# Kernel tuning notes

Measured on AMD Instinct MI355X. Metric: run time of the kernel, lower is better.

The kernel has to match this reference:

```python
import jax, jax.numpy as jnp
import numpy as np

N, E = 20000, 320000
IN_CH, HID, NPRED = 64, 512, 12
NUM_GCN = 3   # num_gcn_layers=4 -> 1 + (4-2) layers
NUM_RNN = 2
BN_EPS = 1e-5


def setup_inputs() -> dict:
    key = jax.random.key(0)
    ks = jax.random.split(key, 16)
    s = 0.05  # init scale to keep activations sane
    return {
        "x": jax.random.normal(ks[0], (N, IN_CH), jnp.float32),
        "edge_index": jax.random.randint(ks[1], (2, E), 0, N, jnp.int32),
        "edge_weight": jax.random.uniform(ks[2], (E,), jnp.float32),
        "gcn0_W": jax.random.normal(ks[3], (IN_CH, HID), jnp.float32) * s,
        "gcn0_b": jnp.zeros((HID,), jnp.float32),
        "gcn_W": jax.random.normal(ks[4], (NUM_GCN - 1, HID, HID), jnp.float32) * s,
        "gcn_b": jnp.zeros((NUM_GCN - 1, HID), jnp.float32),
        "bn_gamma": jnp.ones((NUM_GCN, HID), jnp.float32),
        "bn_beta": jnp.zeros((NUM_GCN, HID), jnp.float32),
        "w_ih": jax.random.normal(ks[5], (NUM_RNN, HID, 4 * HID), jnp.float32) * s,
        "w_hh": jax.random.normal(ks[6], (NUM_RNN, HID, 4 * HID), jnp.float32) * s,
        "w_ch": jax.random.normal(ks[7], (NUM_RNN, HID, 3 * HID), jnp.float32) * s,
        "lstm_b": jnp.zeros((NUM_RNN, 4 * HID), jnp.float32),
        "out_W": jax.random.normal(ks[8], (HID, NPRED), jnp.float32) * s,
        "out_b": jnp.zeros((NPRED,), jnp.float32),
    }


def _gcn(x, W, b, src, dst, ew, n):
    h = x @ W                                   # [N, out]
    msg = ew[:, None] * h[src]                  # [E, out]
    return jax.ops.segment_sum(msg, dst, num_segments=n) + b


def _bn_relu(x, gamma, beta):
    mu = jnp.mean(x, axis=0)
    var = jnp.var(x, axis=0)
    return jax.nn.relu((x - mu) * jax.lax.rsqrt(var + BN_EPS) * gamma + beta)


def _peephole_cell(inp, h, c, Wih, Whh, Wch, b):
    H = h.shape[1]
    gates = inp @ Wih + h @ Whh + b             # [N, 4H]
    i_g, f_g, g_g, o_g = jnp.split(gates, 4, axis=1)
    g_g = g_g + c @ Wch[:, :H]
    i_g = jax.nn.sigmoid(i_g)
    f_g = jax.nn.sigmoid(f_g + c @ Wch[:, H:2 * H])
    g_g = jnp.tanh(g_g)
    cy = f_g * c + i_g * g_g
    o_g = o_g + cy @ Wch[:, 2 * H:]
    hy = jax.nn.sigmoid(o_g) * jnp.tanh(cy)
    return hy, cy


def reference(x, edge_index, edge_weight, gcn0_W, gcn0_b, gcn_W, gcn_b,
              bn_gamma, bn_beta, w_ih, w_hh, w_ch, lstm_b, out_W, out_b):
    src, dst = edge_index[0], edge_index[1]
    n = x.shape[0]
    # GCN stack: conv -> batchnorm (train-mode stats) -> relu (dropout=0)
    h = _gcn(x, gcn0_W, gcn0_b, src, dst, edge_weight, n)
    h = _bn_relu(h, bn_gamma[0], bn_beta[0])
    for i in range(NUM_GCN - 1):
        h = _gcn(h, gcn_W[i], gcn_b[i], src, dst, edge_weight, n)
        h = _bn_relu(h, bn_gamma[i + 1], bn_beta[i + 1])
    # seq_len == 1 after unsqueeze; cells chained sharing (h_t, c_t)
    h_t = jnp.zeros((n, HID), h.dtype)
    c_t = jnp.zeros((n, HID), h.dtype)
    for l in range(NUM_RNN):
        h_t, c_t = _peephole_cell(h, h_t, c_t, w_ih[l], w_hh[l], w_ch[l], lstm_b[l])
    out = h_t @ out_W + out_b                   # [N, num_predictions]
    return jnp.squeeze(out)
```

## Files before the change

### kernel.cpp

```cpp
#include <hip/hip_runtime.h>
#include <cstddef>

#define N_NODES 20000
#define N_EDGES 320000
#define IN_CH   64
#define HID     512
#define G4      2048
#define BN_EPS  1e-5f

typedef __attribute__((ext_vector_type(8))) __bf16 bf16x8;
typedef __attribute__((ext_vector_type(4))) float f32x4;

__device__ __forceinline__ float sigmoidf_(float x) {
  return 1.0f / (1.0f + expf(-x));
}

__device__ __forceinline__ unsigned short f2b(float f) {
  unsigned int u = __float_as_uint(f);
  u += 0x7FFFu + ((u >> 16) & 1u);
  return (unsigned short)(u >> 16);
}
__device__ __forceinline__ float b2f(unsigned short u) {
  return __uint_as_float(((unsigned int)u) << 16);
}

__device__ __forceinline__ void gld_lds16(const unsigned short* g, unsigned short* l) {
  __builtin_amdgcn_global_load_lds(
      (const __attribute__((address_space(1))) unsigned int*)(const void*)g,
      (__attribute__((address_space(3))) unsigned int*)(void*)l, 16, 0, 0);
}

__global__ __launch_bounds__(256) void zero_k(float* __restrict__ p, size_t n) {
  size_t i = ((size_t)blockIdx.x * 256 + threadIdx.x) * 4;
  if (i + 3 < n) {
    *(float4*)&p[i] = make_float4(0.f, 0.f, 0.f, 0.f);
  } else {
    for (; i < n; i++) p[i] = 0.f;
  }
}

__global__ __launch_bounds__(256) void cvt_k(const float* __restrict__ in,
                                             unsigned short* __restrict__ out, size_t n) {
  size_t i = ((size_t)blockIdx.x * 256 + threadIdx.x) * 4;
  if (i + 3 < n) {
    const float4 v = *(const float4*)&in[i];
    ushort4 o; o.x = f2b(v.x); o.y = f2b(v.y); o.z = f2b(v.z); o.w = f2b(v.w);
    *(ushort4*)&out[i] = o;
  } else {
    for (; i < n; i++) out[i] = f2b(in[i]);
  }
}

struct TcvtDesc { const float* W; unsigned short* Wt; int K, NC, ldw, ldo, gate; };
struct TcvtBatch { TcvtDesc d[19]; };

__global__ void tcvtb_k(TcvtBatch batch) {
  const TcvtDesc dd = batch.d[blockIdx.z];
  __shared__ float tile[32][33];
  const int n0 = blockIdx.x * 32, k0 = blockIdx.y * 32;
  if (n0 >= dd.NC || k0 >= dd.K) return;
  const int tx = threadIdx.x, ty = threadIdx.y;
  #pragma unroll
  for (int i = 0; i < 32; i += 8) {
    int k = k0 + ty + i, n = n0 + tx;
    tile[ty + i][tx] = (k < dd.K && n < dd.NC) ? dd.W[(size_t)k * dd.ldw + n] : 0.f;
  }
  __syncthreads();
  #pragma unroll
  for (int i = 0; i < 32; i += 8) {
    int n = n0 + ty + i, k = k0 + tx;
    if (n < dd.NC && k < dd.K) {
      size_t orow = (dd.gate < 0)
          ? (size_t)n
          : (size_t)((n >> 4) * 64 + dd.gate * 16 + (n & 15));
      dd.Wt[orow * dd.ldo + k] = f2b(tile[tx][ty + i]);
    }
  }
}

__global__ __launch_bounds__(256) void hist_k(const int* __restrict__ dst,
                                              int* __restrict__ counts) {
  int e = blockIdx.x * 256 + threadIdx.x;
  if (e < N_EDGES) atomicAdd(&counts[dst[e]], 1);
}

__global__ __launch_bounds__(1024) void scan_k(const int* __restrict__ counts,
                                               int* __restrict__ offsets,
                                               int* __restrict__ pos, int n) {
  __shared__ int tmp[1024];
  __shared__ int carry_s;
  const int tid = threadIdx.x;
  if (tid == 0) carry_s = 0;
  __syncthreads();
  for (int base = 0; base < n; base += 1024) {
    int i = base + tid;
    int v = (i < n) ? counts[i] : 0;
    tmp[tid] = v;
    __syncthreads();
    #pragma unroll
    for (int off = 1; off < 1024; off <<= 1) {
      int t = (tid >= off) ? tmp[tid - off] : 0;
      __syncthreads();
      tmp[tid] += t;
      __syncthreads();
    }
    if (i < n) {
      int excl = carry_s + tmp[tid] - v;
      offsets[i] = excl;
      pos[i] = excl;
    }
    __syncthreads();
    if (tid == 1023) carry_s += tmp[1023];
    __syncthreads();
  }
  if (tid == 0) offsets[n] = carry_s;
}

__global__ __launch_bounds__(256) void fill_k(
    const int* __restrict__ src, const int* __restrict__ dst,
    const float* __restrict__ ew, int* __restrict__ pos,
    int* __restrict__ s_s, float* __restrict__ w_s) {
  int e = blockIdx.x * 256 + threadIdx.x;
  if (e >= N_EDGES) return;
  int p = atomicAdd(&pos[dst[e]], 1);
  s_s[p] = src[e];
  w_s[p] = ew[e];
}

__global__ __launch_bounds__(64) void gather64_k(
    const unsigned short* __restrict__ x16, const int* __restrict__ offsets,
    const int* __restrict__ s_s, const float* __restrict__ w_s,
    unsigned short* __restrict__ xg) {
  const int sub = threadIdx.x >> 4;
  const int cg  = threadIdx.x & 15;
  const int n   = blockIdx.x * 4 + sub;
  const int beg = offsets[n], end = offsets[n + 1];
  float4 acc = make_float4(0.f, 0.f, 0.f, 0.f);
  for (int i = beg; i < end; i++) {
    const int   s = s_s[i];
    const float w = w_s[i];
    const ushort4 v = *(const ushort4*)&x16[(size_t)s * IN_CH + cg * 4];
    acc.x = fmaf(w, b2f(v.x), acc.x);
    acc.y = fmaf(w, b2f(v.y), acc.y);
    acc.z = fmaf(w, b2f(v.z), acc.z);
    acc.w = fmaf(w, b2f(v.w), acc.w);
  }
  ushort4 o; o.x = f2b(acc.x); o.y = f2b(acc.y); o.z = f2b(acc.z); o.w = f2b(acc.w);
  *(ushort4*)&xg[(size_t)n * IN_CH + cg * 4] = o;
}

__global__ __launch_bounds__(128) void gather_k(
    const unsigned short* __restrict__ XW, const int* __restrict__ offsets,
    const int* __restrict__ s_s, const float* __restrict__ w_s,
    unsigned short* __restrict__ H) {
  const int n = blockIdx.x;
  const int t = threadIdx.x;
  const int beg = offsets[n], end = offsets[n + 1];
  float4 acc = make_float4(0.f, 0.f, 0.f, 0.f);
  for (int i = beg; i < end; i++) {
    const int   s = s_s[i];
    const float w = w_s[i];
    const ushort4 v = *(const ushort4*)&XW[(size_t)s * HID + t * 4];
    acc.x = fmaf(w, b2f(v.x), acc.x);
    acc.y = fmaf(w, b2f(v.y), acc.y);
    acc.z = fmaf(w, b2f(v.z), acc.z);
    acc.w = fmaf(w, b2f(v.w), acc.w);
  }
  ushort4 o; o.x = f2b(acc.x); o.y = f2b(acc.y); o.z = f2b(acc.z); o.w = f2b(acc.w);
  *(ushort4*)&H[(size_t)n * HID + t * 4] = o;
}

__global__ __launch_bounds__(256) void bn_stats_k(
    const unsigned short* __restrict__ H, float* __restrict__ stats, int N)
{
  const int tx = threadIdx.x & 63;
  const int ty = threadIdx.x >> 6;
  const int col = blockIdx.x * 64 + tx;
  float s1 = 0.f, s2 = 0.f;
  for (int r = blockIdx.y * 4 + ty; r < N; r += gridDim.y * 4) {
    float v = b2f(H[(size_t)r * HID + col]);
    s1 += v; s2 += v * v;
  }
  __shared__ float red[2][4][64];
  red[0][ty][tx] = s1;
  red[1][ty][tx] = s2;
  __syncthreads();
  if (ty == 0) {
    s1 = red[0][0][tx] + red[0][1][tx] + red[0][2][tx] + red[0][3][tx];
    s2 = red[1][0][tx] + red[1][1][tx] + red[1][2][tx] + red[1][3][tx];
    atomicAdd(&stats[col], s1);
    atomicAdd(&stats[HID + col], s2);
  }
}

__global__ __launch_bounds__(256) void bn_apply_k(
    const unsigned short* __restrict__ H, const float* __restrict__ stats,
    const float* __restrict__ gamma, const float* __restrict__ beta,
    unsigned short* __restrict__ out, int N)
{
  size_t gid = (size_t)blockIdx.x * 256 + threadIdx.x;
  size_t idx = gid * 4;
  if (idx >= (size_t)N * HID) return;
  int col = (int)(idx & (HID - 1));
  const ushort4 v = *(const ushort4*)&H[idx];
  float r[4] = {b2f(v.x), b2f(v.y), b2f(v.z), b2f(v.w)};
  ushort4 o;
  unsigned short* op = &o.x;
  #pragma unroll
  for (int i = 0; i < 4; i++) {
    int c = col + i;
    float mean = stats[c] * (1.0f / N);
    float var  = stats[HID + c] * (1.0f / N) - mean * mean;
    float scale = gamma[c] / sqrtf(var + BN_EPS);
    float shift = beta[c] - mean * scale;
    op[i] = f2b(fmaxf(fmaf(r[i], scale, shift), 0.0f));
  }
  *(ushort4*)&out[idx] = o;
}

template<int BM, int BN>
__global__ __launch_bounds__(256) void gemm_bf16_k(
    const unsigned short* __restrict__ A, int lda,
    const unsigned short* __restrict__ A2, int lda2, int ksplit,
    const unsigned short* __restrict__ Bt,
    float* __restrict__ C, unsigned short* __restrict__ C16,
    const float* __restrict__ bias,
    int M, int K, int Ksmall, int NC, int ldc, int acc, int nrowb, int ncolb)
{
  const int b   = blockIdx.x;
  const int xcd = b & 7;
  const int j   = b >> 3;
  const int col_b = j % ncolb;
  const int row_b = (j / ncolb) * 8 + xcd;
  if (row_b >= nrowb) return;

  constexpr int MI  = 2;
  constexpr int ASZ = BM * 64;
  constexpr int BSZ = BN * 64;
  __shared__ unsigned short As[2 * ASZ];
  __shared__ unsigned short Bs[2 * BSZ];
  const int row0 = row_b * BM;
  const int col0 = col_b * BN;
  const int Kthis = (col0 < 1024) ? K : Ksmall;
  const int t    = threadIdx.x;
  const int lane = t & 63;
  const int w    = t >> 6;
  const int wro  = (BN == 128) ? (w >> 1) * 32 : w * 32;
  const int wco  = (BN == 128) ? (w & 1) * 64 : 0;
  const int q    = lane >> 4;
  const int l16  = lane & 15;

  f32x4 accr[MI][4] = {};

  auto stage = [&](int buf, int k0) {
    unsigned short* Ad = As + buf * ASZ;
    unsigned short* Bd = Bs + buf * BSZ;
    #pragma unroll
    for (int i = 0; i < BM / 32; i++) {
      int s  = t + i * 256;
      int r  = s >> 3, cq = s & 7;
      int kq = (cq - r) & 7;
      int gr = row0 + r; if (gr > M - 1) gr = M - 1;
      int kk = k0 + kq * 8;
      const unsigned short* bp = (kk < ksplit) ? A : A2;
      size_t off = (kk < ksplit) ? ((size_t)gr * lda + kk)
                                 : ((size_t)gr * lda2 + (kk - ksplit));
      gld_lds16(bp + off, Ad + (size_t)s * 8);
    }
    #pragma unroll
    for (int i = 0; i < BN / 32; i++) {
      int s  = t + i * 256;
      int r  = s >> 3, cq = s & 7;
      int kq = (cq - r) & 7;
      gld_lds16(Bt + (size_t)(col0 + r) * K + k0 + kq * 8, Bd + (size_t)s * 8);
    }
  };

  stage(0, 0);
  int cur = 0;
  for (int k0 = 0; k0 < Kthis; k0 += 64) {
    __syncthreads();
    if (k0 + 64 < Kthis) stage(cur ^ 1, k0 + 64);

    const unsigned short* Ac = As + cur * ASZ;
    const unsigned short* Bc = Bs + cur * BSZ;
    #pragma unroll
    for (int ks = 0; ks < 2; ks++) {
      bf16x8 af[MI], bfr[4];
      #pragma unroll
      for (int mi = 0; mi < MI; mi++) {
        int r = wro + mi * 16 + l16;
        int slot = (ks * 4 + q + r) & 7;
        af[mi] = *(const bf16x8*)&Ac[r * 64 + slot * 8];
      }
      #pragma unroll
      for (int ni = 0; ni < 4; ni++) {
        int r = wco + ni * 16 + l16;
        int slot = (ks * 4 + q + r) & 7;
        bfr[ni] = *(const bf16x8*)&Bc[r * 64 + slot * 8];
      }
      #pragma unroll
      for (int mi = 0; mi < MI; mi++)
        #pragma unroll
        for (int ni = 0; ni < 4; ni++)
          accr[mi][ni] = __builtin_amdgcn_mfma_f32_16x16x32_bf16(
              af[mi], bfr[ni], accr[mi][ni], 0, 0, 0);
    }
    cur ^= 1;
  }

  #pragma unroll
  for (int mi = 0; mi < MI; mi++) {
    #pragma unroll
    for (int ni = 0; ni < 4; ni++) {
      int col = col0 + wco + ni * 16 + l16;
      #pragma unroll
      for (int r = 0; r < 4; r++) {
        int row = row0 + wro + mi * 16 + q * 4 + r;
        if (row < M) {
          float v = accr[mi][ni][r];
          if (C16) {
            C16[(size_t)row * ldc + col] = f2b(v);
          } else {
            float* cp = &C[(size_t)row * ldc + col];
            if (acc)       *cp += v;
            else if (bias) *cp  = v + bias[col];
            else           *cp  = v;
          }
        }
      }
    }
  }
}

__global__ __launch_bounds__(256) void gemm_gates_k(
    const unsigned short* __restrict__ A, int lda,
    const unsigned short* __restrict__ A2, int lda2, int ksplit,
    const unsigned short* __restrict__ Bt,
    const float* __restrict__ lb, const float* __restrict__ cin,
    float* __restrict__ cbuf, unsigned short* __restrict__ c16, int ldc16,
    float* __restrict__ ogat,
    int M, int K, int Ksmall, int nrowb)
{
  const int b   = blockIdx.x;
  const int xcd = b & 7;
  const int j   = b >> 3;
  const int col_b = j & 15;
  const int row_b = (j >> 4) * 8 + xcd;
  if (row_b >= nrowb) return;

  constexpr int ASZ = 64 * 64;
  constexpr int BSZ = 128 * 64;
  __shared__ unsigned short As[2 * ASZ];
  __shared__ unsigned short Bs[2 * BSZ];
  const int row0 = row_b * 64;
  const int col0 = col_b * 128;
  const int t    = threadIdx.x;
  const int lane = t & 63;
  const int w    = t >> 6;
  const int wro  = (w >> 1) * 32;
  const int wco  = (w & 1) * 64;
  const int q    = lane >> 4;
  const int l16  = lane & 15;

  f32x4 accr[2][4] = {};

  auto stage = [&](int buf, int k0) {
    unsigned short* Ad = As + buf * ASZ;
    unsigned short* Bd = Bs + buf * BSZ;
    #pragma unroll
    for (int i = 0; i < 2; i++) {
      int s  = t + i * 256;
      int r  = s >> 3, cq = s & 7;
      int kq = (cq - r) & 7;
      int gr = row0 + r; if (gr > M - 1) gr = M - 1;
      int kk = k0 + kq * 8;
      const unsigned short* bp = (kk < ksplit) ? A : A2;
      size_t off = (kk < ksplit) ? ((size_t)gr * lda + kk)
                                 : ((size_t)gr * lda2 + (kk - ksplit));
      gld_lds16(bp + off, Ad + (size_t)s * 8);
    }
    #pragma unroll
    for (int i = 0; i < 4; i++) {
      int s  = t + i * 256;
      int r  = s >> 3, cq = s & 7;
      int kq = (cq - r) & 7;
      gld_lds16(Bt + (size_t)(col0 + r) * K + k0 + kq * 8, Bd + (size_t)s * 8);
    }
  };

  stage(0, 0);
  int cur = 0;
  for (int k0 = 0; k0 < K; k0 += 64) {
    __syncthreads();
    if (k0 + 64 < K) stage(cur ^ 1, k0 + 64);

    const unsigned short* Ac = As + cur * ASZ;
    const unsigned short* Bc = Bs + cur * BSZ;
    const bool full = (k0 < Ksmall);
    #pragma unroll
    for (int ks = 0; ks < 2; ks++) {
      bf16x8 af[2];
      #pragma unroll
      for (int mi = 0; mi < 2; mi++) {
        int r = wro + mi * 16 + l16;
        int slot = (ks * 4 + q + r) & 7;
        af[mi] = *(const bf16x8*)&Ac[r * 64 + slot * 8];
      }
      bf16x8 bfr[4];
      #pragma unroll
      for (int ni = 0; ni < 2; ni++) {
        int r = wco + ni * 16 + l16;
        int slot = (ks * 4 + q + r) & 7;
        bfr[ni] = *(const bf16x8*)&Bc[r * 64 + slot * 8];
      }
      #pragma unroll
      for (int mi = 0; mi < 2; mi++)
        #pragma unroll
        for (int ni = 0; ni < 2; ni++)
          accr[mi][ni] = __builtin_amdgcn_mfma_f32_16x16x32_bf16(
              af[mi], bfr[ni], accr[mi][ni], 0, 0, 0);
      if (full) {
        #pragma unroll
        for (int ni = 2; ni < 4; ni++) {
          int r = wco + ni * 16 + l16;
          int slot = (ks * 4 + q + r) & 7;
          bfr[ni] = *(const bf16x8*)&Bc[r * 64 + slot * 8];
        }
        #pragma unroll
        for (int mi = 0; mi < 2; mi++)
          #pragma unroll
          for (int ni = 2; ni < 4; ni++)
            accr[mi][ni] = __builtin_amdgcn_mfma_f32_16x16x32_bf16(
                af[mi], bfr[ni], accr[mi][ni], 0, 0, 0);
      }
    }
    cur ^= 1;
  }

  const int hgrp = (col0 + wco) >> 6;
  const int h    = hgrp * 16 + l16;
  const float bi  = lb[h];
  const float bfv = lb[HID + h];
  const float bg  = lb[2 * HID + h];
  #pragma unroll
  for (int mi = 0; mi < 2; mi++) {
    #pragma unroll
    for (int r = 0; r < 4; r++) {
      int row = row0 + wro + mi * 16 + q * 4 + r;
      if (row < M) {
        float fv = accr[mi][0][r], gv = accr[mi][1][r];
        float iv = accr[mi][2][r], ov = accr[mi][3][r];
        float ig = sigmoidf_(iv + bi);
        float gg = tanhf(gv + bg);
        float c  = cin ? sigmoidf_(fv + bfv) * cin[(size_t)row * HID + h] + ig * gg
                       : ig * gg;
        cbuf[(size_t)row * HID + h] = c;
        c16[(size_t)row * ldc16 + h] = f2b(c);
        ogat[(size_t)row * HID + h] = ov;
      }
    }
  }
}

__global__ __launch_bounds__(256) void cell2_k(
    const float* __restrict__ ogat, const float* __restrict__ obuf,
    const float* __restrict__ lb, const float* __restrict__ cy,
    unsigned short* __restrict__ hy16, int ld16, int rows)
{
  size_t gid = (size_t)blockIdx.x * 256 + threadIdx.x;
  if (gid >= (size_t)rows * HID) return;
  size_t row = gid >> 9;
  int    col = (int)(gid & (HID - 1));
  float og = sigmoidf_(ogat[gid] + obuf[gid] + lb[3 * HID + col]);
  float h = og * tanhf(cy[gid]);
  hy16[row * ld16 + col] = f2b(h);
}

__global__ __launch_bounds__(256) void cellout_k(
    const float* __restrict__ ogat, const float* __restrict__ obuf,
    const float* __restrict__ lb, const float* __restrict__ cy,
    const float* __restrict__ W, const float* __restrict__ b,
    float* __restrict__ out, int rows)
{
  int wave = (int)(((size_t)blockIdx.x * 256 + threadIdx.x) >> 6);
  int lane = threadIdx.x & 63;
  if (wave >= rows) return;
  const float* g  = &ogat[(size_t)wave * HID];
  const float* ob = &obuf[(size_t)wave * HID];
  const float* cr = &cy[(size_t)wave * HID];
  float hy[8];
  #pragma unroll
  for (int j = 0; j < 8; j++) {
    int k = lane + j * 64;
    float og = sigmoidf_(g[k] + ob[k] + lb[3 * HID + k]);
    hy[j] = og * tanhf(cr[k]);
  }
  float acc[12] = {};
  #pragma unroll
  for (int j = 0; j < 8; j++) {
    int k = lane + j * 64;
    const float* wr = &W[k * 12];
    #pragma unroll
    for (int p = 0; p < 12; p++) acc[p] = fmaf(hy[j], wr[p], acc[p]);
  }
  #pragma unroll
  for (int p = 0; p < 12; p++) {
    float v = acc[p];
    #pragma unroll
    for (int off = 32; off > 0; off >>= 1) v += __shfl_down(v, off);
    if (lane == 0) out[(size_t)wave * 12 + p] = v + b[p];
  }
}

extern "C" void kernel_launch(void* const* d_in, const int* in_sizes, int n_in,
                              void* d_out, int out_size, void* d_ws, size_t ws_size,
                              hipStream_t stream) {
  const float* x     = (const float*)d_in[0];
  const int*   ei    = (const int*)d_in[1];
  const float* ew    = (const float*)d_in[2];
  const float* gcn0W = (const float*)d_in[3];
  const float* gcnW  = (const float*)d_in[5];
  const float* gamma = (const float*)d_in[7];
  const float* beta  = (const float*)d_in[8];
  const float* wih   = (const float*)d_in[9];
  const float* whh   = (const float*)d_in[10];
  const float* wch   = (const float*)d_in[11];
  const float* lstmb = (const float*)d_in[12];
  const float* outW  = (const float*)d_in[13];
  const float* outb  = (const float*)d_in[14];
  float* out = (float*)d_out;

  const int* src = ei;
  const int* dst = ei + N_EDGES;

  const int CH = (ws_size >= (size_t)215000000) ? 10000 : 5000;
  const int NCHUNK = N_NODES / CH;

  const size_t NH = (size_t)N_NODES * HID;
  float* ws = (float*)d_ws;
  float* gates = ws;
  float* bufH  = gates + (size_t)CH * G4;
  unsigned short* hbA16 = (unsigned short*)(bufH + NH);
  unsigned short* hbB16 = hbA16 + NH;
  unsigned short* x16   = hbB16 + NH;
  unsigned short* g0t   = x16 + (size_t)N_NODES * IN_CH;
  unsigned short* g1t   = g0t   + 512 * 64;
  unsigned short* g2t   = g1t   + 512 * 512;
  unsigned short* wih0t = g2t   + 512 * 512;
  unsigned short* wcat3 = wih0t + (size_t)2048 * 512;
  unsigned short* wch0ot= wcat3 + (size_t)2048 * 1536;
  unsigned short* wch1ot= wch0ot + 512 * 512;
  unsigned short* wend  = wch1ot + 512 * 512;
  unsigned short *a16, *c16o, *tail16;
  if (CH == 5000) {
    a16  = hbB16;
    c16o = a16 + (size_t)CH * 1024;
    tail16 = wend;
  } else {
    a16  = wend;
    c16o = a16 + (size_t)CH * 1024;
    tail16 = c16o + (size_t)CH * 512;
  }
  float* stats = (float*)tail16;
  int*   csr   = (int*)(stats + 3072);
  int*   counts  = csr;
  int*   offsets = csr + 20032;
  int*   cpos    = csr + 40064;
  int*   s_s     = csr + 60096;
  float* w_s     = (float*)(csr + 380096);

  unsigned short* bufH16 = (unsigned short*)bufH;
  float* cbuf = bufH;
  float* obuf = bufH + (size_t)CH * HID;
  float* ogat = gates;

  const dim3 blk(256);
  auto gemm_gates = [&](const unsigned short* A, int lda,
                        const unsigned short* A2, int lda2, int ksplit,
                        const unsigned short* Bt, const float* lb,
                        const float* cin, float* cb, unsigned short* c16,
                        int ldc16, int M, int K, int Ksmall) {
    int nrowb = (M + 63) / 64;
    int nblocks = 8 * ((nrowb + 7) / 8) * 16;
    hipLaunchKernelGGL(gemm_gates_k, dim3(nblocks), blk, 0, stream,
                       A, lda, A2, lda2, ksplit, Bt, lb, cin, cb, c16, ldc16,
                       ogat, M, K, Ksmall, nrowb);
  };
  auto gemm64 = [&](const unsigned short* A, int lda,
                    const unsigned short* Bt, float* C, unsigned short* C16,
                    const float* bias, int M, int K, int NC, int ldc, int acc) {
    int nrowb = (M + 127) / 128;
    int ncolb = NC / 64;
    int nblocks = 8 * ((nrowb + 7) / 8) * ncolb;
    hipLaunchKernelGGL((gemm_bf16_k<128, 64>), dim3(nblocks), blk, 0, stream,
                       A, lda, A, lda, K, Bt, C, C16, bias,
                       M, K, K, NC, ldc, acc, nrowb, ncolb);
  };
  auto zero = [&](float* p, size_t n) {
    hipLaunchKernelGGL(zero_k, dim3((unsigned)((n / 4 + 255) / 256)), blk, 0, stream, p, n);
  };

  const float* wih1 = wih + (size_t)HID * G4;
  const float* whh1 = whh + (size_t)HID * G4;
  const float* wch1 = wch + (size_t)HID * 3 * HID;
  {
    TcvtBatch tb;
    int n = 0;
    auto add = [&](const float* W, unsigned short* Wt, int K, int NC, int ldw,
                   int ldo, int gate) {
      tb.d[n++] = TcvtDesc{W, Wt, K, NC, ldw, ldo, gate};
    };
    add(gcn0W, g0t, IN_CH, HID, HID, IN_CH, -1);
    add(gcnW,                     g1t, HID, HID, HID, HID, -1);
    add(gcnW + (size_t)HID * HID, g2t, HID, HID, HID, HID, -1);
    add(wih + HID,     wih0t, HID, HID, G4, HID, 0);
    add(wih + 2 * HID, wih0t, HID, HID, G4, HID, 1);
    add(wih,           wih0t, HID, HID, G4, HID, 2);
    add(wih + 3 * HID, wih0t, HID, HID, G4, HID, 3);
    add(wih1 + HID,     wcat3,        HID, HID, G4,      1536, 0);
    add(whh1 + HID,     wcat3 + 512,  HID, HID, G4,      1536, 0);
    add(wch1 + HID,     wcat3 + 1024, HID, HID, 3 * HID, 1536, 0);
    add(wih1 + 2 * HID, wcat3,        HID, HID, G4,      1536, 1);
    add(whh1 + 2 * HID, wcat3 + 512,  HID, HID, G4,      1536, 1);
    add(wch1,           wcat3 + 1024, HID, HID, 3 * HID, 1536, 1);
    add(wih1,           wcat3,        HID, HID, G4,      1536, 2);
    add(whh1,           wcat3 + 512,  HID, HID, G4,      1536, 2);
    add(wih1 + 3 * HID, wcat3,        HID, HID, G4,      1536, 3);
    add(whh1 + 3 * HID, wcat3 + 512,  HID, HID, G4,      1536, 3);
    add(wch + 2 * HID,  wch0ot, HID, HID, 3 * HID, HID, -1);
    add(wch1 + 2 * HID, wch1ot, HID, HID, 3 * HID, HID, -1);
    hipLaunchKernelGGL(tcvtb_k, dim3(16, 16, 19), dim3(32, 8), 0, stream, tb);
  }
  hipLaunchKernelGGL(cvt_k, dim3((N_NODES * IN_CH / 4 + 255) / 256), blk, 0, stream,
                     x, x16, (size_t)N_NODES * IN_CH);

  const int e_blocks = (N_EDGES + 255) / 256;
  zero((float*)counts, N_NODES);
  zero(stats, 3 * 1024);
  hipLaunchKernelGGL(hist_k, dim3(e_blocks), blk, 0, stream, dst, counts);
  hipLaunchKernelGGL(scan_k, dim3(1), dim3(1024), 0, stream, counts, offsets, cpos, N_NODES);
  hipLaunchKernelGGL(fill_k, dim3(e_blocks), blk, 0, stream, src, dst, ew, cpos, s_s, w_s);

  hipLaunchKernelGGL(gather64_k, dim3(N_NODES / 4), dim3(64), 0, stream,
                     x16, offsets, s_s, w_s, hbB16);
  gemm64(hbB16, IN_CH, g0t, nullptr, bufH16, nullptr, N_NODES, IN_CH, HID, HID, 0);
  hipLaunchKernelGGL(bn_stats_k, dim3(8, 64), blk, 0, stream, bufH16, stats, N_NODES);
  hipLaunchKernelGGL(bn_apply_k, dim3((unsigned)(NH / 4 / 256)), blk, 0, stream,
                     bufH16, stats, gamma, beta, hbA16, N_NODES);

  const unsigned short* gWt2[2] = {g1t, g2t};
  const unsigned short* gA2[2]  = {hbA16, hbB16};
  unsigned short*       gXW2[2] = {hbB16, hbA16};
  unsigned short*       gO2[2]  = {hbB16, hbA16};
  for (int l = 0; l < 2; l++) {
    gemm64(gA2[l], HID, gWt2[l], nullptr, gXW2[l], nullptr, N_NODES, HID, HID, HID, 0);
    hipLaunchKernelGGL(gather_k, dim3(N_NODES), dim3(128), 0, stream,
                       gXW2[l], offsets, s_s, w_s, bufH16);
    hipLaunchKernelGGL(bn_stats_k, dim3(8, 64), blk, 0, stream, bufH16,
                       stats + (l + 1) * 1024, N_NODES);
    hipLaunchKernelGGL(bn_apply_k, dim3((unsigned)(NH / 4 / 256)), blk, 0, stream,
                       bufH16, stats + (l + 1) * 1024, gamma + (l + 1) * HID,
                       beta + (l + 1) * HID, gO2[l], N_NODES);
  }
  unsigned short* hfin16 = hbA16;

  for (int ci = 0; ci < NCHUNK; ci++) {
    const int r0 = ci * CH;
    const unsigned short* h_c = hfin16 + (size_t)r0 * HID;
    const int cell_blocks = (int)(((size_t)CH * HID + 255) / 256);

    gemm_gates(h_c, HID, h_c, HID, HID, wih0t, lstmb, nullptr,
               cbuf, a16 + 512, 1024, CH, HID, HID);
    gemm64(a16 + 512, 1024, wch0ot, obuf, nullptr, nullptr, CH, HID, HID, HID, 0);
    hipLaunchKernelGGL(cell2_k, dim3(cell_blocks), blk, 0, stream,
                       ogat, obuf, lstmb, cbuf, a16, 1024, CH);

    gemm_gates(h_c, HID, a16, 1024, HID, wcat3, lstmb + G4, cbuf,
               cbuf, c16o, 512, CH, 3 * HID, 1024);
    gemm64(c16o, 512, wch1ot, obuf, nullptr, nullptr, CH, HID, HID, HID, 0);
    hipLaunchKernelGGL(cellout_k, dim3((CH * 64 + 255) / 256), blk, 0, stream,
                       ogat, obuf, lstmb + G4, cbuf, outW, outb,
                       out + (size_t)r0 * 12, CH);
  }
}
```

Baseline: 892.9 us.

## Fuse output-gate peephole GEMM with cell epilogue and split output projection

Replaces the generic peephole GEMM plus separate elementwise cell kernels with a dedicated GEMM whose epilogue adds the o-gate partial, applies sigmoid and tanh(c), and writes h as bf16. This removes the fp32 obuf round trip and the separate elementwise launches. The final layer now writes h in bf16 to a scratch buffer and a lighter projection kernel reads it. The B-fragment loads in the gates GEMM are also hoisted out of the conditional. The output projection now uses bf16-rounded h, which adds a small precision change, and it needs an extra bf16 write and read of h.

```diff
diff --git a/kernel.cpp b/kernel.cpp
--- a/kernel.cpp
+++ b/kernel.cpp
@@ -400,16 +400,15 @@
     const bool full = (k0 < Ksmall);
     #pragma unroll
     for (int ks = 0; ks < 2; ks++) {
-      bf16x8 af[2];
+      bf16x8 af[2], bfr[4];
       #pragma unroll
       for (int mi = 0; mi < 2; mi++) {
         int r = wro + mi * 16 + l16;
         int slot = (ks * 4 + q + r) & 7;
         af[mi] = *(const bf16x8*)&Ac[r * 64 + slot * 8];
       }
-      bf16x8 bfr[4];
-      #pragma unroll
-      for (int ni = 0; ni < 2; ni++) {
+      #pragma unroll
+      for (int ni = 0; ni < 4; ni++) {
         int r = wco + ni * 16 + l16;
         int slot = (ks * 4 + q + r) & 7;
         bfr[ni] = *(const bf16x8*)&Bc[r * 64 + slot * 8];
@@ -421,12 +420,6 @@
           accr[mi][ni] = __builtin_amdgcn_mfma_f32_16x16x32_bf16(
               af[mi], bfr[ni], accr[mi][ni], 0, 0, 0);
       if (full) {
-        #pragma unroll
-        for (int ni = 2; ni < 4; ni++) {
-          int r = wco + ni * 16 + l16;
-          int slot = (ks * 4 + q + r) & 7;
-          bfr[ni] = *(const bf16x8*)&Bc[r * 64 + slot * 8];
-        }
         #pragma unroll
         for (int mi = 0; mi < 2; mi++)
           #pragma unroll
@@ -463,44 +456,127 @@
   }
 }
 
-__global__ __launch_bounds__(256) void cell2_k(
-    const float* __restrict__ ogat, const float* __restrict__ obuf,
-    const float* __restrict__ lb, const float* __restrict__ cy,
-    unsigned short* __restrict__ hy16, int ld16, int rows)
+__global__ __launch_bounds__(256) void gemm_peep_k(
+    const unsigned short* __restrict__ A, int lda,
+    const unsigned short* __restrict__ Bt,
+    const float* __restrict__ ogat, const float* __restrict__ lb,
+    const float* __restrict__ cy,
+    unsigned short* __restrict__ hy16, int ldh,
+    int M, int nrowb)
 {
-  size_t gid = (size_t)blockIdx.x * 256 + threadIdx.x;
-  if (gid >= (size_t)rows * HID) return;
-  size_t row = gid >> 9;
-  int    col = (int)(gid & (HID - 1));
-  float og = sigmoidf_(ogat[gid] + obuf[gid] + lb[3 * HID + col]);
-  float h = og * tanhf(cy[gid]);
-  hy16[row * ld16 + col] = f2b(h);
-}
-
-__global__ __launch_bounds__(256) void cellout_k(
-    const float* __restrict__ ogat, const float* __restrict__ obuf,
-    const float* __restrict__ lb, const float* __restrict__ cy,
+  const int b   = blockIdx.x;
+  const int xcd = b & 7;
+  const int j   = b >> 3;
+  const int col_b = j & 7;
+  const int row_b = (j >> 3) * 8 + xcd;
+  if (row_b >= nrowb) return;
+
+  constexpr int K   = 512;
+  constexpr int ASZ = 128 * 64;
+  constexpr int BSZ = 64 * 64;
+  __shared__ unsigned short As[2 * ASZ];
+  __shared__ unsigned short Bs[2 * BSZ];
+  const int row0 = row_b * 128;
+  const int col0 = col_b * 64;
+  const int t    = threadIdx.x;
+  const int lane = t & 63;
+  const int w    = t >> 6;
+  const int wro  = w * 32;
+  const int q    = lane >> 4;
+  const int l16  = lane & 15;
+
+  f32x4 accr[2][4] = {};
+
+  auto stage = [&](int buf, int k0) {
+    unsigned short* Ad = As + buf * ASZ;
+    unsigned short* Bd = Bs + buf * BSZ;
+    #pragma unroll
+    for (int i = 0; i < 4; i++) {
+      int s  = t + i * 256;
+      int r  = s >> 3, cq = s & 7;
+      int kq = (cq - r) & 7;
+      int gr = row0 + r; if (gr > M - 1) gr = M - 1;
+      gld_lds16(A + (size_t)gr * lda + k0 + kq * 8, Ad + (size_t)s * 8);
+    }
+    #pragma unroll
+    for (int i = 0; i < 2; i++) {
+      int s  = t + i * 256;
+      int r  = s >> 3, cq = s & 7;
+      int kq = (cq - r) & 7;
+      gld_lds16(Bt + (size_t)(col0 + r) * K + k0 + kq * 8, Bd + (size_t)s * 8);
+    }
+  };
+
+  stage(0, 0);
+  int cur = 0;
+  for (int k0 = 0; k0 < K; k0 += 64) {
+    __syncthreads();
+    if (k0 + 64 < K) stage(cur ^ 1, k0 + 64);
+
+    const unsigned short* Ac = As + cur * ASZ;
+    const unsigned short* Bc = Bs + cur * BSZ;
+    #pragma unroll
+    for (int ks = 0; ks < 2; ks++) {
+      bf16x8 af[2], bfr[4];
+      #pragma unroll
+      for (int mi = 0; mi < 2; mi++) {
+        int r = wro + mi * 16 + l16;
+        int slot = (ks * 4 + q + r) & 7;
+        af[mi] = *(const bf16x8*)&Ac[r * 64 + slot * 8];
+      }
+      #pragma unroll
+      for (int ni = 0; ni < 4; ni++) {
+        int r = ni * 16 + l16;
+        int slot = (ks * 4 + q + r) & 7;
+        bfr[ni] = *(const bf16x8*)&Bc[r * 64 + slot * 8];
+      }
+      #pragma unroll
+      for (int mi = 0; mi < 2; mi++)
+        #pragma unroll
+        for (int ni = 0; ni < 4; ni++)
+          accr[mi][ni] = __builtin_amdgcn_mfma_f32_16x16x32_bf16(
+              af[mi], bfr[ni], accr[mi][ni], 0, 0, 0);
+    }
+    cur ^= 1;
+  }
+
+  #pragma unroll
+  for (int mi = 0; mi < 2; mi++) {
+    #pragma unroll
+    for (int ni = 0; ni < 4; ni++) {
+      int col = col0 + ni * 16 + l16;
+      const float bo = lb[3 * HID + col];
+      #pragma unroll
+      for (int r = 0; r < 4; r++) {
+        int row = row0 + wro + mi * 16 + q * 4 + r;
+        if (row < M) {
+          size_t ix = (size_t)row * HID + col;
+          float og = sigmoidf_(accr[mi][ni][r] + ogat[ix] + bo);
+          float hv = og * tanhf(cy[ix]);
+          hy16[(size_t)row * ldh + col] = f2b(hv);
+        }
+      }
+    }
+  }
+}
+
+__global__ __launch_bounds__(256) void proj_k(
+    const unsigned short* __restrict__ hy16,
     const float* __restrict__ W, const float* __restrict__ b,
     float* __restrict__ out, int rows)
 {
   int wave = (int)(((size_t)blockIdx.x * 256 + threadIdx.x) >> 6);
   int lane = threadIdx.x & 63;
   if (wave >= rows) return;
-  const float* g  = &ogat[(size_t)wave * HID];
-  const float* ob = &obuf[(size_t)wave * HID];
-  const float* cr = &cy[(size_t)wave * HID];
-  float hy[8];
-  #pragma unroll
-  for (int j = 0; j < 8; j++) {
-    int k = lane + j * 64;
-    float og = sigmoidf_(g[k] + ob[k] + lb[3 * HID + k]);
-    hy[j] = og * tanhf(cr[k]);
-  }
+  const unsigned short* hr = &hy16[(size_t)wave * HID];
+  const ushort4 v0 = *(const ushort4*)&hr[lane * 8];
+  const ushort4 v1 = *(const ushort4*)&hr[lane * 8 + 4];
+  float hy[8] = {b2f(v0.x), b2f(v0.y), b2f(v0.z), b2f(v0.w),
+                 b2f(v1.x), b2f(v1.y), b2f(v1.z), b2f(v1.w)};
   float acc[12] = {};
   #pragma unroll
   for (int j = 0; j < 8; j++) {
-    int k = lane + j * 64;
-    const float* wr = &W[k * 12];
+    const float* wr = &W[(lane * 8 + j) * 12];
     #pragma unroll
     for (int p = 0; p < 12; p++) acc[p] = fmaf(hy[j], wr[p], acc[p]);
   }
@@ -572,8 +648,8 @@
 
   unsigned short* bufH16 = (unsigned short*)bufH;
   float* cbuf = bufH;
-  float* obuf = bufH + (size_t)CH * HID;
   float* ogat = gates;
+  unsigned short* hyb16 = (unsigned short*)(gates + (size_t)CH * 512);
 
   const dim3 blk(256);
   auto gemm_gates = [&](const unsigned short* A, int lda,
@@ -586,6 +662,14 @@
     hipLaunchKernelGGL(gemm_gates_k, dim3(nblocks), blk, 0, stream,
                        A, lda, A2, lda2, ksplit, Bt, lb, cin, cb, c16, ldc16,
                        ogat, M, K, Ksmall, nrowb);
+  };
+  auto gemm_peep = [&](const unsigned short* A, int lda,
+                       const unsigned short* Bt, const float* lb,
+                       unsigned short* hy, int ldh, int M) {
+    int nrowb = (M + 127) / 128;
+    int nblocks = 8 * ((nrowb + 7) / 8) * 8;
+    hipLaunchKernelGGL(gemm_peep_k, dim3(nblocks), blk, 0, stream,
+                       A, lda, Bt, ogat, lb, cbuf, hy, ldh, M, nrowb);
   };
   auto gemm64 = [&](const unsigned short* A, int lda,
                     const unsigned short* Bt, float* C, unsigned short* C16,
@@ -625,7 +709,7 @@
     add(whh1 + 2 * HID, wcat3 + 512,  HID, HID, G4,      1536, 1);
     add(wch1,           wcat3 + 1024, HID, HID, 3 * HID, 1536, 1);
     add(wih1,           wcat3,        HID, HID, G4,      1536, 2);
-    add(whh1,           wcat3 + 512,  HID, HID, G4,      1536, 2);
+    add(whh1 + 0,       wcat3 + 512,  HID, HID, G4,      1536, 2);
     add(wih1 + 3 * HID, wcat3,        HID, HID, G4,      1536, 3);
     add(whh1 + 3 * HID, wcat3 + 512,  HID, HID, G4,      1536, 3);
     add(wch + 2 * HID,  wch0ot, HID, HID, 3 * HID, HID, -1);
@@ -668,19 +752,15 @@
   for (int ci = 0; ci < NCHUNK; ci++) {
     const int r0 = ci * CH;
     const unsigned short* h_c = hfin16 + (size_t)r0 * HID;
-    const int cell_blocks = (int)(((size_t)CH * HID + 255) / 256);
 
     gemm_gates(h_c, HID, h_c, HID, HID, wih0t, lstmb, nullptr,
                cbuf, a16 + 512, 1024, CH, HID, HID);
-    gemm64(a16 + 512, 1024, wch0ot, obuf, nullptr, nullptr, CH, HID, HID, HID, 0);
-    hipLaunchKernelGGL(cell2_k, dim3(cell_blocks), blk, 0, stream,
-                       ogat, obuf, lstmb, cbuf, a16, 1024, CH);
+    gemm_peep(a16 + 512, 1024, wch0ot, lstmb, a16, 1024, CH);
 
     gemm_gates(h_c, HID, a16, 1024, HID, wcat3, lstmb + G4, cbuf,
                cbuf, c16o, 512, CH, 3 * HID, 1024);
-    gemm64(c16o, 512, wch1ot, obuf, nullptr, nullptr, CH, HID, HID, HID, 0);
-    hipLaunchKernelGGL(cellout_k, dim3((CH * 64 + 255) / 256), blk, 0, stream,
-                       ogat, obuf, lstmb + G4, cbuf, outW, outb,
-                       out + (size_t)r0 * 12, CH);
-  }
-}
+    gemm_peep(c16o, 512, wch1ot, lstmb + G4, hyb16, 512, CH);
+    hipLaunchKernelGGL(proj_k, dim3((CH * 64 + 255) / 256), blk, 0, stream,
+                       hyb16, outW, outb, out + (size_t)r0 * 12, CH);
+  }
+}
```

After: 928.6 us. 1.04x slower.
